# Performance work log

Hardware: AMD Instinct MI355X
Metric: run time of the kernel (lower is better)

## Reference

```python
import jax, jax.numpy as jnp
import numpy as np

N_A, N_B = 50000, 200000          # coarse / fine active voxel counts
C_A, C_B, C_OUT = 256, 128, 256   # channels: x_a, x_b (skip), output
K_T, M_T = 8, 100000              # transpose conv: 2^3 offsets, pairs per offset
K_C, M_C = 27, 120000             # 3x3x3 conv: 27 offsets, pairs per offset
EPS = 1e-5


def setup_inputs() -> dict:
    key = jax.random.key(0)
    ks = jax.random.split(key, 12)
    feats_a = jax.random.normal(ks[0], (N_A, C_A), jnp.float32)
    feats_b = jax.random.normal(ks[1], (N_B, C_B), jnp.float32)
    W_t = jax.random.normal(ks[2], (K_T, C_A, C_A), jnp.float32) * 0.05
    W_c = jax.random.normal(ks[3], (K_C, C_A + C_B, C_OUT), jnp.float32) * 0.05
    in_map_t = jax.random.randint(ks[4], (K_T, M_T), 0, N_A, dtype=jnp.int32)
    out_map_t = jax.random.randint(ks[5], (K_T, M_T), 0, N_B, dtype=jnp.int32)
    in_map_c = jax.random.randint(ks[6], (K_C, M_C), 0, N_B, dtype=jnp.int32)
    out_map_c = jax.random.randint(ks[7], (K_C, M_C), 0, N_B, dtype=jnp.int32)
    bn_t_gamma = jax.random.uniform(ks[8], (C_A,), jnp.float32, 0.5, 1.5)
    bn_t_beta = jax.random.normal(ks[9], (C_A,), jnp.float32) * 0.1
    bn_t_mean = jax.random.normal(ks[10], (C_A,), jnp.float32) * 0.1
    bn_t_var = jax.random.uniform(ks[11], (C_A,), jnp.float32, 0.5, 1.5)
    k2 = jax.random.split(jax.random.key(1), 4)
    bn_c_gamma = jax.random.uniform(k2[0], (C_OUT,), jnp.float32, 0.5, 1.5)
    bn_c_beta = jax.random.normal(k2[1], (C_OUT,), jnp.float32) * 0.1
    bn_c_mean = jax.random.normal(k2[2], (C_OUT,), jnp.float32) * 0.1
    bn_c_var = jax.random.uniform(k2[3], (C_OUT,), jnp.float32, 0.5, 1.5)
    return {
        "feats_a": feats_a, "feats_b": feats_b,
        "W_t": W_t, "bn_t_gamma": bn_t_gamma, "bn_t_beta": bn_t_beta,
        "bn_t_mean": bn_t_mean, "bn_t_var": bn_t_var,
        "W_c": W_c, "bn_c_gamma": bn_c_gamma, "bn_c_beta": bn_c_beta,
        "bn_c_mean": bn_c_mean, "bn_c_var": bn_c_var,
        "in_map_t": in_map_t, "out_map_t": out_map_t,
        "in_map_c": in_map_c, "out_map_c": out_map_c,
    }


def _sparse_conv(feats, in_map, out_map, W, n_out):
    """MinkowskiEngine gather-GEMM-scatter over kernel maps.
    feats: [N_in, C_in]; in_map/out_map: [K, M] index pairs per kernel offset;
    W: [K, C_in, C_out]. Scan over the K offsets (small fixed set) to keep
    peak memory at one [M, C] slab."""
    acc0 = jnp.zeros((n_out, W.shape[-1]), feats.dtype)

    def step(acc, kmaps):
        im, om, Wk = kmaps
        acc = acc.at[om].add(feats[im] @ Wk)  # gather -> GEMM -> scatter-add
        return acc, None

    out, _ = jax.lax.scan(step, acc0, (in_map, out_map, W))
    return out


def _bn_relu(x, gamma, beta, mean, var):
    # BatchNorm in eval mode (running stats) + ReLU
    return jax.nn.relu((x - mean) * (gamma / jnp.sqrt(var + EPS)) + beta)


def reference(feats_a, feats_b, W_t, bn_t_gamma, bn_t_beta, bn_t_mean, bn_t_var,
              W_c, bn_c_gamma, bn_c_beta, bn_c_mean, bn_c_var,
              in_map_t, out_map_t, in_map_c, out_map_c):
    # conv_a: transpose conv (k=2, s=2) -> BN -> ReLU; output lives on x_b coords
    xa = _sparse_conv(feats_a, in_map_t, out_map_t, W_t, N_B)
    xa = _bn_relu(xa, bn_t_gamma, bn_t_beta, bn_t_mean, bn_t_var)
    # ME.cat: concatenate features at identical coordinates
    x = jnp.concatenate([xa, feats_b], axis=-1)  # [N_B, C_A + C_B]
    # conv_proj: 3x3x3 conv -> BN -> ReLU
    x = _sparse_conv(x, in_map_c, out_map_c, W_c, N_B)
    return _bn_relu(x, bn_c_gamma, bn_c_beta, bn_c_mean, bn_c_var)
```

## Files before the change

### kernel.cpp

```cpp
#include <hip/hip_runtime.h>
#include <hip/hip_bf16.h>
#include <stdint.h>

typedef __attribute__((ext_vector_type(8))) short bf16x8;
typedef __attribute__((ext_vector_type(4))) float floatx4;

#define DEV __device__ __forceinline__

DEV void gl_lds16(const void* g, void* lds) {
    __builtin_amdgcn_global_load_lds(
        (const __attribute__((address_space(1))) unsigned int*)g,
        (__attribute__((address_space(3))) unsigned int*)lds, 16, 0, 0);
}

template <int KSTEPS>
__global__ __launch_bounds__(256) void spconv_kernel(
    const __hip_bfloat16* __restrict__ A, const __hip_bfloat16* __restrict__ BT,
    const int* __restrict__ in_map, const int* __restrict__ out_map,
    float* __restrict__ Out, int M) {
    constexpr int K = KSTEPS * 32;
    __shared__ __align__(16) char Abuf[8192];
    __shared__ __align__(16) char Bbuf[8192];
    __shared__ int om_s[128];

    const int tid = threadIdx.x;
    const int w = tid >> 6;
    const int l = tid & 63;
    const int koff = blockIdx.z;
    const int m0 = blockIdx.x * 128;
    const int n0 = blockIdx.y * 128;

    const int* im = in_map + (size_t)koff * M;
    const int* om = out_map + (size_t)koff * M;

    if (tid < 128) {
        int p = m0 + tid;
        om_s[tid] = (p < M) ? om[p] : -1;
    }

    const int rS = (w & 1) * 64 + l;
    int prow = m0 + rS;
    if (prow > M - 1) prow = M - 1;
    const __hip_bfloat16* a_row = A + (size_t)im[prow] * K;
    const __hip_bfloat16* b_row = BT + ((size_t)koff * 256 + n0 + rS) * (size_t)K;
    const int q0 = w >> 1;

    char* Al = Abuf + w * 1024 + l * 16;
    char* Bl = Bbuf + w * 1024 + l * 16;

    floatx4 acc[4][4];
#pragma unroll
    for (int i = 0; i < 4; i++)
#pragma unroll
        for (int j = 0; j < 4; j++) acc[i][j] = (floatx4)0.0f;

    const int wm = w & 1, wn = w >> 1;
    const int lm = l & 15, lq = l >> 4;

    for (int ks = 0; ks < KSTEPS; ks++) {
        const int kb = ks * 32;
        gl_lds16(a_row + kb + q0 * 8, Al);
        gl_lds16(a_row + kb + (q0 + 2) * 8, Al + 4096);
        gl_lds16(b_row + kb + q0 * 8, Bl);
        gl_lds16(b_row + kb + (q0 + 2) * 8, Bl + 4096);
        __syncthreads();

        bf16x8 af[4], bf[4];
#pragma unroll
        for (int mt = 0; mt < 4; mt++)
            af[mt] = *(const bf16x8*)(Abuf + lq * 2048 + (wm * 64 + mt * 16 + lm) * 16);
#pragma unroll
        for (int nt = 0; nt < 4; nt++)
            bf[nt] = *(const bf16x8*)(Bbuf + lq * 2048 + (wn * 64 + nt * 16 + lm) * 16);

#pragma unroll
        for (int mt = 0; mt < 4; mt++)
#pragma unroll
            for (int nt = 0; nt < 4; nt++)
                acc[mt][nt] = __builtin_amdgcn_mfma_f32_16x16x32_bf16(
                    af[mt], bf[nt], acc[mt][nt], 0, 0, 0);

        __syncthreads();
    }

#pragma unroll
    for (int mt = 0; mt < 4; mt++) {
        const int mbase = wm * 64 + mt * 16 + lq * 4;
#pragma unroll
        for (int r = 0; r < 4; r++) {
            const int orow = om_s[mbase + r];
            if (orow >= 0) {
                float* dst = Out + (size_t)orow * 256 + n0 + wn * 64 + lm;
#pragma unroll
                for (int nt = 0; nt < 4; nt++)
                    unsafeAtomicAdd(dst + nt * 16, acc[mt][nt][r]);
            }
        }
    }
}

struct __align__(8) bf4 { __hip_bfloat16 h[4]; };

__global__ void cast_bf16_kernel(const float* __restrict__ in,
                                 __hip_bfloat16* __restrict__ out, int n4) {
    int stride = gridDim.x * blockDim.x;
    for (int i = blockIdx.x * blockDim.x + threadIdx.x; i < n4; i += stride) {
        float4 v = ((const float4*)in)[i];
        bf4 o;
        o.h[0] = __float2bfloat16(v.x);
        o.h[1] = __float2bfloat16(v.y);
        o.h[2] = __float2bfloat16(v.z);
        o.h[3] = __float2bfloat16(v.w);
        ((bf4*)out)[i] = o;
    }
}

__global__ void transpose_cast_w(const float* __restrict__ W,
                                 __hip_bfloat16* __restrict__ WT, int Koff,
                                 int Cin, int Cout) {
    int total = Koff * Cin * Cout;
    int stride = gridDim.x * blockDim.x;
    for (int i = blockIdx.x * blockDim.x + threadIdx.x; i < total; i += stride) {
        int k = i / (Cin * Cout);
        int r = i - k * (Cin * Cout);
        int n = r / Cin;
        int kk = r - n * Cin;
        WT[i] = __float2bfloat16(W[((size_t)k * Cin + kk) * Cout + n]);
    }
}

__global__ void bn_concat_kernel(const float* __restrict__ xa,
                                 const float* __restrict__ fb,
                                 const float* __restrict__ g,
                                 const float* __restrict__ b,
                                 const float* __restrict__ mu,
                                 const float* __restrict__ var,
                                 __hip_bfloat16* __restrict__ X) {
    const int total = 200000 * 96;
    int stride = gridDim.x * blockDim.x;
    for (int i = blockIdx.x * blockDim.x + threadIdx.x; i < total; i += stride) {
        int row = i / 96;
        int c4 = (i - row * 96) * 4;
        float v[4];
        if (c4 < 256) {
            float4 t = *(const float4*)(xa + (size_t)row * 256 + c4);
            v[0] = t.x; v[1] = t.y; v[2] = t.z; v[3] = t.w;
#pragma unroll
            for (int j = 0; j < 4; j++) {
                int c = c4 + j;
                float s = g[c] * rsqrtf(var[c] + 1e-5f);
                v[j] = fmaxf((v[j] - mu[c]) * s + b[c], 0.0f);
            }
        } else {
            float4 t = *(const float4*)(fb + (size_t)row * 128 + (c4 - 256));
            v[0] = t.x; v[1] = t.y; v[2] = t.z; v[3] = t.w;
        }
        bf4 o;
#pragma unroll
        for (int j = 0; j < 4; j++) o.h[j] = __float2bfloat16(v[j]);
        *(bf4*)(X + (size_t)row * 384 + c4) = o;
    }
}

__global__ void bn_out_kernel(float* __restrict__ out, const float* __restrict__ g,
                              const float* __restrict__ b,
                              const float* __restrict__ mu,
                              const float* __restrict__ var) {
    const int total = 200000 * 64;
    int stride = gridDim.x * blockDim.x;
    for (int i = blockIdx.x * blockDim.x + threadIdx.x; i < total; i += stride) {
        int c4 = (i & 63) * 4;
        float4 t = ((const float4*)out)[i];
        float v[4] = {t.x, t.y, t.z, t.w};
#pragma unroll
        for (int j = 0; j < 4; j++) {
            int c = c4 + j;
            float s = g[c] * rsqrtf(var[c] + 1e-5f);
            v[j] = fmaxf((v[j] - mu[c]) * s + b[c], 0.0f);
        }
        ((float4*)out)[i] = make_float4(v[0], v[1], v[2], v[3]);
    }
}

extern "C" void kernel_launch(void* const* d_in, const int* in_sizes, int n_in,
                              void* d_out, int out_size, void* d_ws,
                              size_t ws_size, hipStream_t stream) {
    const float* feats_a = (const float*)d_in[0];
    const float* feats_b = (const float*)d_in[1];
    const float* W_t = (const float*)d_in[2];
    const float* bn_t_gamma = (const float*)d_in[3];
    const float* bn_t_beta = (const float*)d_in[4];
    const float* bn_t_mean = (const float*)d_in[5];
    const float* bn_t_var = (const float*)d_in[6];
    const float* W_c = (const float*)d_in[7];
    const float* bn_c_gamma = (const float*)d_in[8];
    const float* bn_c_beta = (const float*)d_in[9];
    const float* bn_c_mean = (const float*)d_in[10];
    const float* bn_c_var = (const float*)d_in[11];
    const int* in_map_t = (const int*)d_in[12];
    const int* out_map_t = (const int*)d_in[13];
    const int* in_map_c = (const int*)d_in[14];
    const int* out_map_c = (const int*)d_in[15];
    float* out = (float*)d_out;

    char* ws = (char*)d_ws;
    __hip_bfloat16* a_bf = (__hip_bfloat16*)ws;
    __hip_bfloat16* wtT = (__hip_bfloat16*)(ws + 25600000);
    __hip_bfloat16* wcT = (__hip_bfloat16*)(ws + 26648576);
    __hip_bfloat16* x_bf = (__hip_bfloat16*)(ws + 31956992);

    cast_bf16_kernel<<<512, 256, 0, stream>>>(feats_a, a_bf, 50000 * 256 / 4);
    transpose_cast_w<<<512, 256, 0, stream>>>(W_t, wtT, 8, 256, 256);
    transpose_cast_w<<<512, 256, 0, stream>>>(W_c, wcT, 27, 384, 256);

    hipMemsetAsync(d_out, 0, (size_t)out_size * sizeof(float), stream);
    dim3 g1(782, 2, 8);
    spconv_kernel<8><<<g1, 256, 0, stream>>>(a_bf, wtT, in_map_t, out_map_t, out, 100000);

    bn_concat_kernel<<<2048, 256, 0, stream>>>(out, feats_b, bn_t_gamma, bn_t_beta,
                                               bn_t_mean, bn_t_var, x_bf);

    hipMemsetAsync(d_out, 0, (size_t)out_size * sizeof(float), stream);
    dim3 g2(938, 2, 27);
    spconv_kernel<12><<<g2, 256, 0, stream>>>(x_bf, wcT, in_map_c, out_map_c, out, 120000);

    bn_out_kernel<<<2048, 256, 0, stream>>>(out, bn_c_gamma, bn_c_beta, bn_c_mean,
                                            bn_c_var);
}
```

Before: 4.001 ms.

## Replace atomic scatter-add with staged bf16 partials and CSR gather reduction

The sparse conv is split into two kernels. A GEMM stage writes per-pair results as bf16 into a workspace buffer, processing kernel offsets in groups sized to the available workspace. A gather stage then reduces those partials per output row using a CSR index built from out_map (histogram, scan, scatter), and fuses BN+ReLU (and the concat write) into its last pass. This removes fp32 global atomics, but adds large write/read traffic for the partial buffer, bf16 rounding of partials, and setup kernels. The old atomic path is kept as a fallback when workspace is too small.

```diff
diff --git a/kernel.cpp b/kernel.cpp
--- a/kernel.cpp
+++ b/kernel.cpp
@@ -13,36 +13,30 @@
         (__attribute__((address_space(3))) unsigned int*)lds, 16, 0, 0);
 }
 
+struct __align__(8) bf4 { __hip_bfloat16 h[4]; };
+
 template <int KSTEPS>
-__global__ __launch_bounds__(256) void spconv_kernel(
+__global__ __launch_bounds__(256) void spconv_stage1(
     const __hip_bfloat16* __restrict__ A, const __hip_bfloat16* __restrict__ BT,
-    const int* __restrict__ in_map, const int* __restrict__ out_map,
-    float* __restrict__ Out, int M) {
+    const int* __restrict__ in_map, __hip_bfloat16* __restrict__ P, int M) {
     constexpr int K = KSTEPS * 32;
     __shared__ __align__(16) char Abuf[8192];
     __shared__ __align__(16) char Bbuf[8192];
-    __shared__ int om_s[128];
 
     const int tid = threadIdx.x;
     const int w = tid >> 6;
     const int l = tid & 63;
-    const int koff = blockIdx.z;
+    const int kz = blockIdx.z;
     const int m0 = blockIdx.x * 128;
     const int n0 = blockIdx.y * 128;
 
-    const int* im = in_map + (size_t)koff * M;
-    const int* om = out_map + (size_t)koff * M;
-
-    if (tid < 128) {
-        int p = m0 + tid;
-        om_s[tid] = (p < M) ? om[p] : -1;
-    }
+    const int* im = in_map + (size_t)kz * M;
 
     const int rS = (w & 1) * 64 + l;
     int prow = m0 + rS;
     if (prow > M - 1) prow = M - 1;
     const __hip_bfloat16* a_row = A + (size_t)im[prow] * K;
-    const __hip_bfloat16* b_row = BT + ((size_t)koff * 256 + n0 + rS) * (size_t)K;
+    const __hip_bfloat16* b_row = BT + ((size_t)kz * 256 + n0 + rS) * (size_t)K;
     const int q0 = w >> 1;
 
     char* Al = Abuf + w * 1024 + l * 16;
@@ -83,23 +77,150 @@
         __syncthreads();
     }
 
+    __hip_bfloat16* pbase = P + (size_t)kz * M * 256 + n0 + wn * 64 + lm * 4;
 #pragma unroll
     for (int mt = 0; mt < 4; mt++) {
-        const int mbase = wm * 64 + mt * 16 + lq * 4;
+        const int rowb = wm * 64 + mt * 16 + lq * 4;
 #pragma unroll
         for (int r = 0; r < 4; r++) {
-            const int orow = om_s[mbase + r];
-            if (orow >= 0) {
-                float* dst = Out + (size_t)orow * 256 + n0 + wn * 64 + lm;
+            const int pair = m0 + rowb + r;
+            if (pair < M) {
+                bf4 o;
 #pragma unroll
                 for (int nt = 0; nt < 4; nt++)
-                    unsafeAtomicAdd(dst + nt * 16, acc[mt][nt][r]);
+                    o.h[nt] = __float2bfloat16(acc[mt][nt][r]);
+                *(bf4*)(pbase + (size_t)pair * 256) = o;
             }
         }
     }
 }
 
-struct __align__(8) bf4 { __hip_bfloat16 h[4]; };
+__global__ void stage2_kernel(const unsigned* __restrict__ start,
+                              const unsigned* __restrict__ entries,
+                              const __hip_bfloat16* __restrict__ P,
+                              int kp_lo, int kp_hi,
+                              float* __restrict__ partial, int init, int fin_mode,
+                              __hip_bfloat16* __restrict__ xbf,
+                              float* __restrict__ outp,
+                              const float* __restrict__ g, const float* __restrict__ b,
+                              const float* __restrict__ mu, const float* __restrict__ var) {
+    const int tid = threadIdx.x;
+    const int r = blockIdx.x * 4 + (tid >> 6);
+    const int l = tid & 63;
+    const int pos0 = l * 4;
+
+    float acc[4];
+    if (init) {
+        acc[0] = acc[1] = acc[2] = acc[3] = 0.0f;
+    } else {
+        const float4 t = *(const float4*)(partial + (size_t)r * 256 + pos0);
+        acc[0] = t.x; acc[1] = t.y; acc[2] = t.z; acc[3] = t.w;
+    }
+
+    const unsigned s0 = start[r], s1 = start[r + 1];
+    for (unsigned e = s0; e < s1; ++e) {
+        const int kp = (int)entries[e];
+        if (kp >= kp_lo && kp < kp_hi) {
+            const bf4 v = *(const bf4*)(P + (size_t)(kp - kp_lo) * 256 + pos0);
+#pragma unroll
+            for (int j = 0; j < 4; j++) acc[j] += __bfloat162float(v.h[j]);
+        }
+    }
+
+    if (fin_mode == 0) {
+        *(float4*)(partial + (size_t)r * 256 + pos0) =
+            make_float4(acc[0], acc[1], acc[2], acc[3]);
+    } else {
+        const int chunk = l >> 4, lm = l & 15;
+#pragma unroll
+        for (int j = 0; j < 4; j++) {
+            const int c = chunk * 64 + j * 16 + lm;
+            const float s = g[c] * rsqrtf(var[c] + 1e-5f);
+            const float val = fmaxf((acc[j] - mu[c]) * s + b[c], 0.0f);
+            if (fin_mode == 1)
+                xbf[(size_t)r * 384 + c] = __float2bfloat16(val);
+            else
+                outp[(size_t)r * 256 + c] = val;
+        }
+    }
+}
+
+__global__ void hist_kernel(const int* __restrict__ om, int n,
+                            unsigned* __restrict__ cnt) {
+    int stride = gridDim.x * blockDim.x;
+    for (int i = blockIdx.x * blockDim.x + threadIdx.x; i < n; i += stride)
+        atomicAdd(&cnt[om[i]], 1u);
+}
+
+__global__ void scan1_kernel(const unsigned* __restrict__ cnt,
+                             unsigned* __restrict__ start,
+                             unsigned* __restrict__ bsum, int N) {
+    __shared__ unsigned sums[256];
+    const int t = threadIdx.x;
+    const int base = blockIdx.x * 1024 + t * 4;
+    unsigned v[4];
+#pragma unroll
+    for (int j = 0; j < 4; j++) v[j] = (base + j < N) ? cnt[base + j] : 0u;
+    const unsigned T = v[0] + v[1] + v[2] + v[3];
+    sums[t] = T;
+    __syncthreads();
+    for (int off = 1; off < 256; off <<= 1) {
+        unsigned x = (t >= off) ? sums[t - off] : 0u;
+        __syncthreads();
+        sums[t] += x;
+        __syncthreads();
+    }
+    unsigned run = sums[t] - T;
+#pragma unroll
+    for (int j = 0; j < 4; j++) {
+        if (base + j < N) start[base + j] = run;
+        run += v[j];
+    }
+    if (t == 255) bsum[blockIdx.x] = sums[255];
+}
+
+__global__ void scan2_kernel(unsigned* bsum, int nb) {
+    __shared__ unsigned sums[256];
+    const int t = threadIdx.x;
+    const unsigned v = (t < nb) ? bsum[t] : 0u;
+    sums[t] = v;
+    __syncthreads();
+    for (int off = 1; off < 256; off <<= 1) {
+        unsigned x = (t >= off) ? sums[t - off] : 0u;
+        __syncthreads();
+        sums[t] += x;
+        __syncthreads();
+    }
+    if (t < nb) bsum[t] = sums[t] - v;
+}
+
+__global__ void scan3_kernel(unsigned* __restrict__ start,
+                             const unsigned* __restrict__ bsum,
+                             unsigned* __restrict__ cursor, int N, unsigned total) {
+    const int t = threadIdx.x;
+    const int base = blockIdx.x * 1024 + t * 4;
+    const unsigned add = bsum[blockIdx.x];
+#pragma unroll
+    for (int j = 0; j < 4; j++) {
+        const int i = base + j;
+        if (i < N) {
+            const unsigned s = start[i] + add;
+            start[i] = s;
+            cursor[i] = s;
+        }
+    }
+    if (blockIdx.x == gridDim.x - 1 && t == 255) start[N] = total;
+}
+
+__global__ void scatter_kernel(const int* __restrict__ om, int n,
+                               unsigned* __restrict__ cursor,
+                               unsigned* __restrict__ entries) {
+    int stride = gridDim.x * blockDim.x;
+    for (int i = blockIdx.x * blockDim.x + threadIdx.x; i < n; i += stride) {
+        unsigned pos = atomicAdd(&cursor[om[i]], 1u);
+        entries[pos] = (unsigned)i;
+    }
+}
 
 __global__ void cast_bf16_kernel(const float* __restrict__ in,
                                  __hip_bfloat16* __restrict__ out, int n4) {
@@ -126,6 +247,109 @@
         int n = r / Cin;
         int kk = r - n * Cin;
         WT[i] = __float2bfloat16(W[((size_t)k * Cin + kk) * Cout + n]);
+    }
+}
+
+__global__ void concat_b_kernel(const float* __restrict__ fb,
+                                __hip_bfloat16* __restrict__ X) {
+    const int total = 200000 * 32;
+    int stride = gridDim.x * blockDim.x;
+    for (int i = blockIdx.x * blockDim.x + threadIdx.x; i < total; i += stride) {
+        int row = i >> 5;
+        int c4 = (i & 31) * 4;
+        float4 t = *(const float4*)(fb + (size_t)row * 128 + c4);
+        bf4 o;
+        o.h[0] = __float2bfloat16(t.x);
+        o.h[1] = __float2bfloat16(t.y);
+        o.h[2] = __float2bfloat16(t.z);
+        o.h[3] = __float2bfloat16(t.w);
+        *(bf4*)(X + (size_t)row * 384 + 256 + c4) = o;
+    }
+}
+
+template <int KSTEPS>
+__global__ __launch_bounds__(256) void spconv_atomic(
+    const __hip_bfloat16* __restrict__ A, const __hip_bfloat16* __restrict__ BT,
+    const int* __restrict__ in_map, const int* __restrict__ out_map,
+    float* __restrict__ Out, int M) {
+    constexpr int K = KSTEPS * 32;
+    __shared__ __align__(16) char Abuf[8192];
+    __shared__ __align__(16) char Bbuf[8192];
+    __shared__ int om_s[128];
+
+    const int tid = threadIdx.x;
+    const int w = tid >> 6;
+    const int l = tid & 63;
+    const int koff = blockIdx.z;
+    const int m0 = blockIdx.x * 128;
+    const int n0 = blockIdx.y * 128;
+
+    const int* im = in_map + (size_t)koff * M;
+    const int* om = out_map + (size_t)koff * M;
+
+    if (tid < 128) {
+        int p = m0 + tid;
+        om_s[tid] = (p < M) ? om[p] : -1;
+    }
+
+    const int rS = (w & 1) * 64 + l;
+    int prow = m0 + rS;
+    if (prow > M - 1) prow = M - 1;
+    const __hip_bfloat16* a_row = A + (size_t)im[prow] * K;
+    const __hip_bfloat16* b_row = BT + ((size_t)koff * 256 + n0 + rS) * (size_t)K;
+    const int q0 = w >> 1;
+
+    char* Al = Abuf + w * 1024 + l * 16;
+    char* Bl = Bbuf + w * 1024 + l * 16;
+
+    floatx4 acc[4][4];
+#pragma unroll
+    for (int i = 0; i < 4; i++)
+#pragma unroll
+        for (int j = 0; j < 4; j++) acc[i][j] = (floatx4)0.0f;
+
+    const int wm = w & 1, wn = w >> 1;
+    const int lm = l & 15, lq = l >> 4;
+
+    for (int ks = 0; ks < KSTEPS; ks++) {
+        const int kb = ks * 32;
+        gl_lds16(a_row + kb + q0 * 8, Al);
+        gl_lds16(a_row + kb + (q0 + 2) * 8, Al + 4096);
+        gl_lds16(b_row + kb + q0 * 8, Bl);
+        gl_lds16(b_row + kb + (q0 + 2) * 8, Bl + 4096);
+        __syncthreads();
+
+        bf16x8 af[4], bf[4];
+#pragma unroll
+        for (int mt = 0; mt < 4; mt++)
+            af[mt] = *(const bf16x8*)(Abuf + lq * 2048 + (wm * 64 + mt * 16 + lm) * 16);
+#pragma unroll
+        for (int nt = 0; nt < 4; nt++)
+            bf[nt] = *(const bf16x8*)(Bbuf + lq * 2048 + (wn * 64 + nt * 16 + lm) * 16);
+
+#pragma unroll
+        for (int mt = 0; mt < 4; mt++)
+#pragma unroll
+            for (int nt = 0; nt < 4; nt++)
+                acc[mt][nt] = __builtin_amdgcn_mfma_f32_16x16x32_bf16(
+                    af[mt], bf[nt], acc[mt][nt], 0, 0, 0);
+
+        __syncthreads();
+    }
+
+#pragma unroll
+    for (int mt = 0; mt < 4; mt++) {
+        const int mbase = wm * 64 + mt * 16 + lq * 4;
+#pragma unroll
+        for (int r = 0; r < 4; r++) {
+            const int orow = om_s[mbase + r];
+            if (orow >= 0) {
+                float* dst = Out + (size_t)orow * 256 + n0 + wn * 64 + lm;
+#pragma unroll
+                for (int nt = 0; nt < 4; nt++)
+                    unsafeAtomicAdd(dst + nt * 16, acc[mt][nt][r]);
+            }
+        }
     }
 }
 
@@ -204,26 +428,79 @@
     float* out = (float*)d_out;
 
     char* ws = (char*)d_ws;
-    __hip_bfloat16* a_bf = (__hip_bfloat16*)ws;
-    __hip_bfloat16* wtT = (__hip_bfloat16*)(ws + 25600000);
-    __hip_bfloat16* wcT = (__hip_bfloat16*)(ws + 26648576);
+    __hip_bfloat16* a_bf = (__hip_bfloat16*)(ws + 0);
+    __hip_bfloat16* wtT  = (__hip_bfloat16*)(ws + 25600000);
+    __hip_bfloat16* wcT  = (__hip_bfloat16*)(ws + 26648576);
     __hip_bfloat16* x_bf = (__hip_bfloat16*)(ws + 31956992);
+    unsigned* cnt   = (unsigned*)(ws + 185556992);
+    unsigned* start = (unsigned*)(ws + 186356992);
+    unsigned* bsum  = (unsigned*)(ws + 187157248);
+    unsigned* cur   = (unsigned*)(ws + 187158272);
+    unsigned* ent   = (unsigned*)(ws + 187958272);
+    __hip_bfloat16* P = (__hip_bfloat16*)(ws + 200918272);
+    const size_t p_avail = (ws_size > 200918272u) ? ws_size - 200918272u : 0;
+    int g_c = (int)(p_avail / 61440000ull); if (g_c > 27) g_c = 27;
+    int g_t = (int)(p_avail / 51200000ull); if (g_t > 8) g_t = 8;
+    const bool ts_t = (g_t >= 4);
+    const bool ts_c = (g_c >= 5);
 
     cast_bf16_kernel<<<512, 256, 0, stream>>>(feats_a, a_bf, 50000 * 256 / 4);
     transpose_cast_w<<<512, 256, 0, stream>>>(W_t, wtT, 8, 256, 256);
     transpose_cast_w<<<512, 256, 0, stream>>>(W_c, wcT, 27, 384, 256);
 
-    hipMemsetAsync(d_out, 0, (size_t)out_size * sizeof(float), stream);
-    dim3 g1(782, 2, 8);
-    spconv_kernel<8><<<g1, 256, 0, stream>>>(a_bf, wtT, in_map_t, out_map_t, out, 100000);
-
-    bn_concat_kernel<<<2048, 256, 0, stream>>>(out, feats_b, bn_t_gamma, bn_t_beta,
-                                               bn_t_mean, bn_t_var, x_bf);
-
-    hipMemsetAsync(d_out, 0, (size_t)out_size * sizeof(float), stream);
-    dim3 g2(938, 2, 27);
-    spconv_kernel<12><<<g2, 256, 0, stream>>>(x_bf, wcT, in_map_c, out_map_c, out, 120000);
-
-    bn_out_kernel<<<2048, 256, 0, stream>>>(out, bn_c_gamma, bn_c_beta, bn_c_mean,
-                                            bn_c_var);
-}
+    if (ts_t) {
+        concat_b_kernel<<<2048, 256, 0, stream>>>(feats_b, x_bf);
+        hipMemsetAsync(cnt, 0, 800000, stream);
+        hist_kernel<<<1024, 256, 0, stream>>>(out_map_t, 800000, cnt);
+        scan1_kernel<<<196, 256, 0, stream>>>(cnt, start, bsum, 200000);
+        scan2_kernel<<<1, 256, 0, stream>>>(bsum, 196);
+        scan3_kernel<<<196, 256, 0, stream>>>(start, bsum, cur, 200000, 800000);
+        scatter_kernel<<<1024, 256, 0, stream>>>(out_map_t, 800000, cur, ent);
+        for (int q0 = 0; q0 < 8; q0 += g_t) {
+            const int q1 = (q0 + g_t < 8) ? q0 + g_t : 8;
+            dim3 gs(782, 2, q1 - q0);
+            spconv_stage1<8><<<gs, 256, 0, stream>>>(
+                a_bf, wtT + (size_t)q0 * 256 * 256, in_map_t + (size_t)q0 * 100000,
+                P, 100000);
+            stage2_kernel<<<50000, 256, 0, stream>>>(
+                start, ent, P, q0 * 100000, q1 * 100000, out, (q0 == 0) ? 1 : 0,
+                (q1 == 8) ? 1 : 0, x_bf, out, bn_t_gamma, bn_t_beta, bn_t_mean,
+                bn_t_var);
+        }
+    } else {
+        hipMemsetAsync(d_out, 0, (size_t)out_size * sizeof(float), stream);
+        dim3 g1(782, 2, 8);
+        spconv_atomic<8><<<g1, 256, 0, stream>>>(a_bf, wtT, in_map_t, out_map_t,
+                                                 out, 100000);
+        bn_concat_kernel<<<2048, 256, 0, stream>>>(out, feats_b, bn_t_gamma,
+                                                   bn_t_beta, bn_t_mean, bn_t_var,
+                                                   x_bf);
+    }
+
+    if (ts_c) {
+        hipMemsetAsync(cnt, 0, 800000, stream);
+        hist_kernel<<<1024, 256, 0, stream>>>(out_map_c, 3240000, cnt);
+        scan1_kernel<<<196, 256, 0, stream>>>(cnt, start, bsum, 200000);
+        scan2_kernel<<<1, 256, 0, stream>>>(bsum, 196);
+        scan3_kernel<<<196, 256, 0, stream>>>(start, bsum, cur, 200000, 3240000);
+        scatter_kernel<<<1024, 256, 0, stream>>>(out_map_c, 3240000, cur, ent);
+        for (int q0 = 0; q0 < 27; q0 += g_c) {
+            const int q1 = (q0 + g_c < 27) ? q0 + g_c : 27;
+            dim3 gs(938, 2, q1 - q0);
+            spconv_stage1<12><<<gs, 256, 0, stream>>>(
+                x_bf, wcT + (size_t)q0 * 256 * 384, in_map_c + (size_t)q0 * 120000,
+                P, 120000);
+            stage2_kernel<<<50000, 256, 0, stream>>>(
+                start, ent, P, q0 * 120000, q1 * 120000, out, (q0 == 0) ? 1 : 0,
+                (q1 == 27) ? 2 : 0, x_bf, out, bn_c_gamma, bn_c_beta, bn_c_mean,
+                bn_c_var);
+        }
+    } else {
+        hipMemsetAsync(d_out, 0, (size_t)out_size * sizeof(float), stream);
+        dim3 g2(938, 2, 27);
+        spconv_atomic<12><<<g2, 256, 0, stream>>>(x_bf, wcT, in_map_c, out_map_c,
+                                                  out, 120000);
+        bn_out_kernel<<<2048, 256, 0, stream>>>(out, bn_c_gamma, bn_c_beta,
+                                                bn_c_mean, bn_c_var);
+    }
+}
```

New measurement: 4.130 ms. 3.2% more time.
